# Kernel tuning notes

Hardware: AMD Instinct MI355X
Metric: run time of the kernel (lower is better)

## Reference

```python
import jax, jax.numpy as jnp
import numpy as np

DIMS = 2048
HEADS = 16
HEAD_DIM = DIMS // HEADS  # 128
WIN = 256
THETA = 10000.0


def rotate_half(x):
    x1, x2 = jnp.split(x, 2, axis=-1)
    return jnp.concatenate([-x2, x1], axis=-1)


def rope_freqs(seq_len):
    inv_freq = 1.0 / (THETA ** (jnp.arange(0, HEAD_DIM, 2, dtype=jnp.float32) / HEAD_DIM))
    f = jnp.outer(jnp.arange(seq_len, dtype=jnp.float32), inv_freq)  # [S, D/2]
    return jnp.concatenate([f, f], axis=-1)[None, :, None, :]  # [1, S, 1, D]


def setup_inputs() -> dict:
    key = jax.random.key(0)
    ks = jax.random.split(key, 5)
    B, S = 2, 8192
    scale = 1.0 / np.sqrt(DIMS).astype(np.float32)
    return {
        "hidden_states": jax.random.normal(ks[0], (B, S, DIMS), jnp.float32),
        "Wq": jax.random.normal(ks[1], (DIMS, DIMS), jnp.float32) * scale,
        "Wk": jax.random.normal(ks[2], (DIMS, DIMS), jnp.float32) * scale,
        "Wv": jax.random.normal(ks[3], (DIMS, DIMS), jnp.float32) * scale,
        "Wo": jax.random.normal(ks[4], (DIMS, DIMS), jnp.float32) * scale,
    }


def reference(hidden_states, Wq, Wk, Wv, Wo):
    B, S, _ = hidden_states.shape
    # projections (weights stored [in, out])
    q = (hidden_states @ Wq).reshape(B, S, HEADS, HEAD_DIM)
    k = (hidden_states @ Wk).reshape(B, S, HEADS, HEAD_DIM)
    v = (hidden_states @ Wv).reshape(B, S, HEADS, HEAD_DIM)

    freqs = rope_freqs(S)
    cos, sin = jnp.cos(freqs), jnp.sin(freqs)
    q = q * cos + rotate_half(q) * sin
    k = k * cos + rotate_half(k) * sin

    C = S // WIN
    qc = q.reshape(B, C, WIN, HEADS, HEAD_DIM)
    kc = k.reshape(B, C, WIN, HEADS, HEAD_DIM)
    vc = v.reshape(B, C, WIN, HEADS, HEAD_DIM)

    # previous chunk's K/V (zeros for chunk 0; masked out anyway)
    kp = jnp.concatenate([jnp.zeros_like(kc[:, :1]), kc[:, :-1]], axis=1)
    vp = jnp.concatenate([jnp.zeros_like(vc[:, :1]), vc[:, :-1]], axis=1)
    kcat = jnp.concatenate([kp, kc], axis=2)  # [B, C, 2W, H, D]
    vcat = jnp.concatenate([vp, vc], axis=2)

    scores = jnp.einsum('bcqhd,bckhd->bchqk', qc, kcat) / np.float32(np.sqrt(HEAD_DIM))

    causal = jnp.tril(jnp.ones((WIN, WIN), dtype=bool))  # current-chunk causal
    prev_ok = (jnp.arange(C) > 0)[:, None, None]  # chunk 0 has no previous chunk
    mask = jnp.concatenate([
        jnp.broadcast_to(prev_ok, (C, WIN, WIN)),
        jnp.broadcast_to(causal[None], (C, WIN, WIN)),
    ], axis=-1)  # [C, W, 2W]

    scores = jnp.where(mask[None, :, None], scores, -jnp.inf)
    probs = jax.nn.softmax(scores, axis=-1)
    out = jnp.einsum('bchqk,bckhd->bcqhd', probs, vcat)
    out = out.reshape(B, S, DIMS)
    return out @ Wo
```

## Files before the change

### kernel.cpp

```cpp
#include <hip/hip_runtime.h>
#include <cmath>

#define DIMS 2048
#define SEQ  8192
#define NB   2
#define HEADS 16
#define HD   128
#define WINW 256
#define MROWS 16384
#define NCH  32

using bf16x8 = __attribute__((ext_vector_type(8))) short;
using f32x4  = __attribute__((ext_vector_type(4))) float;

__device__ __forceinline__ unsigned short f2bf(float f) {
  unsigned int u = __float_as_uint(f);
  u += 0x7FFF + ((u >> 16) & 1);
  return (unsigned short)(u >> 16);
}

__device__ __forceinline__ void async16(const unsigned short* g, unsigned short* l) {
  __builtin_amdgcn_global_load_lds((const __attribute__((address_space(1))) void*)g,
                                   (__attribute__((address_space(3))) void*)l,
                                   16, 0, 0);
}

#define BAR() __builtin_amdgcn_s_barrier()
#define WAIT_LGKM0() do { asm volatile("s_waitcnt lgkmcnt(0)" ::: "memory"); \
                          __builtin_amdgcn_sched_barrier(0); } while (0)
#define WAIT_LGKM(n) do { asm volatile("s_waitcnt lgkmcnt(" #n ")" ::: "memory"); \
                          __builtin_amdgcn_sched_barrier(0); } while (0)
#define ORDER() asm volatile("" ::: "memory")
#define WAIT_VM(n) asm volatile("s_waitcnt vmcnt(" #n ")" ::: "memory")
#define MFMA16(a, b, c) __builtin_amdgcn_mfma_f32_16x16x32_bf16(a, b, c, 0, 0, 0)

__global__ __launch_bounds__(256) void prep(
    const float* __restrict__ w0, const float* __restrict__ w1,
    const float* __restrict__ w2, const float* __restrict__ w3,
    const float* __restrict__ H,
    unsigned short* __restrict__ Wt, unsigned short* __restrict__ Hb,
    float* __restrict__ cosT, float* __restrict__ sinT) {
  __shared__ unsigned short tile[64][65];
  const int bid = blockIdx.x;
  const int t = threadIdx.x;
  if (bid < 4096) {
    const int z = bid & 3;
    const int rest = bid >> 2;
    const int n0 = (rest & 31) * 64, k0 = (rest >> 5) * 64;
    const float* W = (z == 0) ? w0 : (z == 1) ? w1 : (z == 2) ? w2 : w3;
    unsigned short* O = Wt + (size_t)z * DIMS * DIMS;
    #pragma unroll
    for (int p = 0; p < 16; ++p) {
      int i = p * 4 + (t >> 6);
      int j = t & 63;
      tile[i][j] = f2bf(W[(size_t)(k0 + i) * DIMS + n0 + j]);
    }
    __syncthreads();
    #pragma unroll
    for (int p = 0; p < 16; ++p) {
      int a = p * 4 + (t >> 6);
      int b = t & 63;
      O[(size_t)(n0 + a) * DIMS + k0 + b] = tile[b][a];
    }
  } else if (bid < 6144) {
    const long n4 = (long)MROWS * DIMS / 4;
    long i = (long)(bid - 4096) * 256 + t;
    for (; i < n4; i += 524288) {
      float4 v = ((const float4*)H)[i];
      ushort4 o;
      o.x = f2bf(v.x); o.y = f2bf(v.y); o.z = f2bf(v.z); o.w = f2bf(v.w);
      ((ushort4*)Hb)[i] = o;
    }
  } else {
    int tl = (bid - 6144) * 256 + t;
    int pos = tl >> 6, i = tl & 63;
    float inv = powf(10000.0f, -(float)i / 64.0f);
    float ang = (float)pos * inv;
    float s, cc;
    __sincosf(ang, &s, &cc);
    cosT[tl] = cc;
    sinT[tl] = s;
  }
}

template<int MODE>
__global__ __launch_bounds__(512, 2) void gemm256(
    const unsigned short* __restrict__ A,
    const unsigned short* __restrict__ WtAll,
    unsigned short* __restrict__ OutB,
    float* __restrict__ OutF,
    const float* __restrict__ cosT,
    const float* __restrict__ sinT) {
  __shared__ __align__(1024) unsigned short lds[65536];
  unsigned short* const As0 = lds;
  unsigned short* const Bs0 = lds + 16384;
  unsigned short* const As1 = lds + 32768;
  unsigned short* const Bs1 = lds + 49152;

  const int tid = threadIdx.x;
  const int wid = tid >> 6, lane = tid & 63;
  const int lo = lane & 15, hi = lane >> 4;
  const int wm = wid >> 2, wn = wid & 3;
  const int flip = (lo & 7) << 4;

  const int nwg = gridDim.x;
  const int orig = blockIdx.x;
  const int bid = (orig & 7) * (nwg >> 3) + (orig >> 3);

  int by, bx, z;
  if (MODE == 0) {
    z = bid >> 9;
    by = (bid & 511) >> 3;
    bx = bid & 7;
  } else {
    by = bid >> 3; bx = bid & 7; z = 3;
  }
  const int m0 = by * 256, n0 = bx * 256;
  const unsigned short* const Ag = A;
  const unsigned short* const Bg = WtAll + (size_t)z * DIMS * DIMS;

  f32x4 acc[8][4];
  #pragma unroll
  for (int i = 0; i < 8; ++i)
    #pragma unroll
    for (int j = 0; j < 4; ++j)
      acc[i][j] = (f32x4){0.f, 0.f, 0.f, 0.f};

  auto stage_half = [&](const unsigned short* __restrict__ G, int grow0, int tile,
                        unsigned short* dst) {
    const int k0 = tile * 64;
    #pragma unroll
    for (int h8 = 0; h8 < 2; ++h8) {
      const int c = h8 * 8 + wid;
      const int row = c * 8 + (lane >> 3);
      const int col8 = (lane & 7) ^ (lane >> 3);
      async16(G + (size_t)(grow0 + row) * DIMS + k0 + col8 * 8, dst + c * 512);
    }
  };
  auto rdA = [&](const unsigned short* base, int i, int kk) -> bf16x8 {
    const int r = i * 32 + wm * 16 + lo;
    const int cb = (kk * 64 + hi * 16) ^ flip;
    return *(const bf16x8*)((const char*)base + r * 128 + cb);
  };
  auto rdB = [&](const unsigned short* base, int j, int kk) -> bf16x8 {
    const int r = j * 64 + wn * 16 + lo;
    const int cb = (kk * 64 + hi * 16) ^ flip;
    return *(const bf16x8*)((const char*)base + r * 128 + cb);
  };

  bf16x8 aq[4][2], b0[2][2], b1[2][2];

  stage_half(Ag, m0,       0, As0);
  stage_half(Bg, n0,       0, Bs0);
  stage_half(Ag, m0 + 128, 0, As0 + 8192);
  stage_half(Bg, n0 + 128, 0, Bs0 + 8192);
  stage_half(Ag, m0,       1, As1);
  stage_half(Bg, n0,       1, Bs1);
  stage_half(Bg, n0 + 128, 1, Bs1 + 8192);
  WAIT_VM(6);
  BAR();

  #pragma unroll 1
  for (int it = 0; it < 16; ++it) {
    const int t = 2 * it;
    const bool pre = (it < 15);
    #pragma unroll
    for (int i = 0; i < 4; ++i) aq[i][0] = rdA(As0, i, 0);
    #pragma unroll
    for (int j = 0; j < 2; ++j) b0[j][0] = rdB(Bs0, j, 0);
    ORDER();
    #pragma unroll
    for (int i = 0; i < 4; ++i) aq[i][1] = rdA(As0, i, 1);
    #pragma unroll
    for (int j = 0; j < 2; ++j) b0[j][1] = rdB(Bs0, j, 1);
    stage_half(Ag, m0 + 128, t + 1, As1 + 8192);
    WAIT_LGKM(6);
    __builtin_amdgcn_s_setprio(1);
    #pragma unroll
    for (int i = 0; i < 4; ++i)
      #pragma unroll
      for (int j = 0; j < 2; ++j)
        acc[i][j] = MFMA16(aq[i][0], b0[j][0], acc[i][j]);
    WAIT_LGKM0();
    #pragma unroll
    for (int i = 0; i < 4; ++i)
      #pragma unroll
      for (int j = 0; j < 2; ++j)
        acc[i][j] = MFMA16(aq[i][1], b0[j][1], acc[i][j]);
    __builtin_amdgcn_s_setprio(0);
    BAR();
    #pragma unroll
    for (int j = 0; j < 2; ++j) b1[j][0] = rdB(Bs0, 2 + j, 0);
    ORDER();
    #pragma unroll
    for (int j = 0; j < 2; ++j) b1[j][1] = rdB(Bs0, 2 + j, 1);
    if (pre) stage_half(Ag, m0, t + 2, As0);
    WAIT_LGKM(2);
    __builtin_amdgcn_s_setprio(1);
    #pragma unroll
    for (int i = 0; i < 4; ++i)
      #pragma unroll
      for (int j = 0; j < 2; ++j)
        acc[i][2 + j] = MFMA16(aq[i][0], b1[j][0], acc[i][2 + j]);
    WAIT_LGKM0();
    #pragma unroll
    for (int i = 0; i < 4; ++i)
      #pragma unroll
      for (int j = 0; j < 2; ++j)
        acc[i][2 + j] = MFMA16(aq[i][1], b1[j][1], acc[i][2 + j]);
    __builtin_amdgcn_s_setprio(0);
    BAR();
    #pragma unroll
    for (int i = 0; i < 4; ++i) aq[i][0] = rdA(As0, 4 + i, 0);
    ORDER();
    #pragma unroll
    for (int i = 0; i < 4; ++i) aq[i][1] = rdA(As0, 4 + i, 1);
    if (pre) stage_half(Bg, n0, t + 2, Bs0);
    WAIT_LGKM(4);
    __builtin_amdgcn_s_setprio(1);
    #pragma unroll
    for (int i = 0; i < 4; ++i)
      #pragma unroll
      for (int j = 0; j < 2; ++j)
        acc[4 + i][j] = MFMA16(aq[i][0], b0[j][0], acc[4 + i][j]);
    WAIT_LGKM0();
    #pragma unroll
    for (int i = 0; i < 4; ++i)
      #pragma unroll
      for (int j = 0; j < 2; ++j)
        acc[4 + i][j] = MFMA16(aq[i][1], b0[j][1], acc[4 + i][j]);
    __builtin_amdgcn_s_setprio(0);
    BAR();
    if (pre) stage_half(Bg, n0 + 128, t + 2, Bs0 + 8192);
    __builtin_amdgcn_s_setprio(1);
    #pragma unroll
    for (int kk = 0; kk < 2; ++kk)
      #pragma unroll
      for (int i = 0; i < 4; ++i)
        #pragma unroll
        for (int j = 0; j < 2; ++j)
          acc[4 + i][2 + j] = MFMA16(aq[i][kk], b1[j][kk], acc[4 + i][2 + j]);
    __builtin_amdgcn_s_setprio(0);
    if (it == 15) { WAIT_VM(0); } else { WAIT_VM(6); }
    BAR();
    #pragma unroll
    for (int i = 0; i < 4; ++i) aq[i][0] = rdA(As1, i, 0);
    #pragma unroll
    for (int j = 0; j < 2; ++j) b0[j][0] = rdB(Bs1, j, 0);
    ORDER();
    #pragma unroll
    for (int i = 0; i < 4; ++i) aq[i][1] = rdA(As1, i, 1);
    #pragma unroll
    for (int j = 0; j < 2; ++j) b0[j][1] = rdB(Bs1, j, 1);
    if (pre) stage_half(Ag, m0 + 128, t + 2, As0 + 8192);
    WAIT_LGKM(6);
    __builtin_amdgcn_s_setprio(1);
    #pragma unroll
    for (int i = 0; i < 4; ++i)
      #pragma unroll
      for (int j = 0; j < 2; ++j)
        acc[i][j] = MFMA16(aq[i][0], b0[j][0], acc[i][j]);
    WAIT_LGKM0();
    #pragma unroll
    for (int i = 0; i < 4; ++i)
      #pragma unroll
      for (int j = 0; j < 2; ++j)
        acc[i][j] = MFMA16(aq[i][1], b0[j][1], acc[i][j]);
    __builtin_amdgcn_s_setprio(0);
    BAR();
    #pragma unroll
    for (int j = 0; j < 2; ++j) b1[j][0] = rdB(Bs1, 2 + j, 0);
    ORDER();
    #pragma unroll
    for (int j = 0; j < 2; ++j) b1[j][1] = rdB(Bs1, 2 + j, 1);
    if (pre) stage_half(Ag, m0, t + 3, As1);
    WAIT_LGKM(2);
    __builtin_amdgcn_s_setprio(1);
    #pragma unroll
    for (int i = 0; i < 4; ++i)
      #pragma unroll
      for (int j = 0; j < 2; ++j)
        acc[i][2 + j] = MFMA16(aq[i][0], b1[j][0], acc[i][2 + j]);
    WAIT_LGKM0();
    #pragma unroll
    for (int i = 0; i < 4; ++i)
      #pragma unroll
      for (int j = 0; j < 2; ++j)
        acc[i][2 + j] = MFMA16(aq[i][1], b1[j][1], acc[i][2 + j]);
    __builtin_amdgcn_s_setprio(0);
    BAR();
    #pragma unroll
    for (int i = 0; i < 4; ++i) aq[i][0] = rdA(As1, 4 + i, 0);
    ORDER();
    #pragma unroll
    for (int i = 0; i < 4; ++i) aq[i][1] = rdA(As1, 4 + i, 1);
    if (pre) stage_half(Bg, n0, t + 3, Bs1);
    WAIT_LGKM(4);
    __builtin_amdgcn_s_setprio(1);
    #pragma unroll
    for (int i = 0; i < 4; ++i)
      #pragma unroll
      for (int j = 0; j < 2; ++j)
        acc[4 + i][j] = MFMA16(aq[i][0], b0[j][0], acc[4 + i][j]);
    WAIT_LGKM0();
    #pragma unroll
    for (int i = 0; i < 4; ++i)
      #pragma unroll
      for (int j = 0; j < 2; ++j)
        acc[4 + i][j] = MFMA16(aq[i][1], b0[j][1], acc[4 + i][j]);
    __builtin_amdgcn_s_setprio(0);
    BAR();
    if (pre) stage_half(Bg, n0 + 128, t + 3, Bs1 + 8192);
    __builtin_amdgcn_s_setprio(1);
    #pragma unroll
    for (int kk = 0; kk < 2; ++kk)
      #pragma unroll
      for (int i = 0; i < 4; ++i)
        #pragma unroll
        for (int j = 0; j < 2; ++j)
          acc[4 + i][2 + j] = MFMA16(aq[i][kk], b1[j][kk], acc[4 + i][2 + j]);
    __builtin_amdgcn_s_setprio(0);
    WAIT_VM(6);
    BAR();
  }

  if (MODE == 0 && z == 2) {
    unsigned short* vt = OutB + (size_t)2 * MROWS * DIMS;
    #pragma unroll
    for (int i = 0; i < 8; ++i) {
      const int row0 = m0 + i * 32 + wm * 16 + hi * 4;
      const int bb = row0 >> 13;
      const int s0 = row0 & (SEQ - 1);
      #pragma unroll
      for (int j = 0; j < 4; ++j) {
        const int colg = n0 + j * 64 + wn * 16 + lo;
        ushort4 pk;
        pk.x = f2bf(acc[i][j][0]); pk.y = f2bf(acc[i][j][1]);
        pk.z = f2bf(acc[i][j][2]); pk.w = f2bf(acc[i][j][3]);
        *(ushort4*)&vt[(((size_t)(bb * 2048 + colg)) << 13) + s0] = pk;
      }
    }
  } else {
    unsigned short* outb = (MODE == 0) ? (OutB + (size_t)z * MROWS * DIMS)
                                       : (unsigned short*)nullptr;
    #pragma unroll
    for (int i = 0; i < 8; ++i) {
      #pragma unroll
      for (int rr = 0; rr < 4; ++rr) {
        const int row = m0 + i * 32 + wm * 16 + hi * 4 + rr;
        const int s = row & (SEQ - 1);
        if (MODE == 1) {
          float* o = OutF + (size_t)row * DIMS + n0;
          #pragma unroll
          for (int j = 0; j < 4; ++j) o[j * 64 + wn * 16 + lo] = acc[i][j][rr];
        } else {
          unsigned short* o = outb + (size_t)row * DIMS + n0;
          const int d = wn * 16 + lo;
          const float cc = cosT[s * 64 + d], sn = sinT[s * 64 + d];
          #pragma unroll
          for (int p = 0; p < 2; ++p) {
            const float v1 = acc[i][2 * p][rr], v2 = acc[i][2 * p + 1][rr];
            o[p * 128 + d]      = f2bf(v1 * cc - v2 * sn);
            o[p * 128 + d + 64] = f2bf(v2 * cc + v1 * sn);
          }
        }
      }
    }
  }
}

__global__ __launch_bounds__(256, 2) void attn(
    const unsigned short* __restrict__ Qb,
    const unsigned short* __restrict__ Kb,
    const unsigned short* __restrict__ Vt,
    unsigned short* __restrict__ AO) {
  __shared__ unsigned short Ksm[2][64 * 128];
  __shared__ unsigned short Vsm[2][128 * 64];
  __shared__ unsigned short Psm[4 * 32 * 64];

  const int nwg = gridDim.x;
  const int orig = blockIdx.x;
  const int bid = (orig & 7) * (nwg >> 3) + (orig >> 3);

  const int qh = bid & 1;
  const int h = (bid >> 1) & 15;
  const int c = (bid >> 5) & 31;
  const int b = bid >> 10;
  const int tid = threadIdx.x;
  const int wid = tid >> 6, lane = tid & 63;
  const int lo = lane & 15, hi = lane >> 4;
  const float SCALE = 0.08838834764831845f;

  const int qbase = qh * 128 + wid * 32;

  bf16x8 qf[2][4];
  {
    const size_t base = ((size_t)(b * SEQ + c * WINW + qbase + lo)) * DIMS + h * HD;
    #pragma unroll
    for (int m = 0; m < 2; ++m)
      #pragma unroll
      for (int ks = 0; ks < 4; ++ks)
        qf[m][ks] = *(const bf16x8*)&Qb[base + (size_t)m * 16 * DIMS + ks * 32 + hi * 8];
  }

  f32x4 O[2][8];
  float mrow[2][4], lrow[2][4];
  #pragma unroll
  for (int m = 0; m < 2; ++m) {
    #pragma unroll
    for (int n = 0; n < 8; ++n) O[m][n] = (f32x4){0.f, 0.f, 0.f, 0.f};
    #pragma unroll
    for (int r = 0; r < 4; ++r) { mrow[m][r] = -INFINITY; lrow[m][r] = 0.f; }
  }

  unsigned short* Pw = Psm + wid * 32 * 64;
  const int t0 = (c == 0) ? 4 : 0;
  const int tend = 5 + 2 * qh;

  const unsigned short* Kg0 = Kb + ((size_t)(b * SEQ + (c - 1) * WINW)) * DIMS + h * HD;
  const unsigned short* Vg0 = Vt + (((size_t)(b * 2048 + h * HD)) << 13) + (c - 1) * WINW;

  auto stageKV = [&](int t, int pb) {
    #pragma unroll
    for (int p = 0; p < 4; ++p) {
      const int cid = p * 256 + tid;
      const int row = cid >> 4, c16 = cid & 15;
      async16(Kg0 + (size_t)(t * 64 + row) * DIMS + ((c16 ^ (row & 7)) << 3),
              &Ksm[pb][cid * 8]);
    }
    #pragma unroll
    for (int p = 0; p < 4; ++p) {
      const int cid = p * 256 + tid;
      const int rd = cid >> 3, c8 = cid & 7;
      async16(Vg0 + ((size_t)rd << 13) + t * 64 + ((c8 ^ (rd & 7)) << 3),
              &Vsm[pb][cid * 8]);
    }
  };

  stageKV(t0, t0 & 1);
  for (int t = t0; t <= tend; ++t) {
    const int pb = t & 1;
    if (t < tend) { stageKV(t + 1, pb ^ 1); WAIT_VM(8); } else { WAIT_VM(0); }
    BAR();

    const bool active = (t < 4) || (((t - 4) << 6) <= qbase + 31);
    if (active) {
      f32x4 S[2][4];
      #pragma unroll
      for (int m = 0; m < 2; ++m)
        #pragma unroll
        for (int n = 0; n < 4; ++n)
          S[m][n] = (f32x4){0.f, 0.f, 0.f, 0.f};
      const char* Kbase = (const char*)&Ksm[pb][0];
      #pragma unroll
      for (int ks = 0; ks < 4; ++ks) {
        bf16x8 kf[4];
        #pragma unroll
        for (int n = 0; n < 4; ++n)
          kf[n] = *(const bf16x8*)(Kbase + (n * 16 + lo) * 256 +
                                   (((ks * 4 + hi) ^ (lo & 7)) << 4));
        #pragma unroll
        for (int m = 0; m < 2; ++m)
          #pragma unroll
          for (int n = 0; n < 4; ++n)
            S[m][n] = MFMA16(qf[m][ks], kf[n], S[m][n]);
      }

      float tmax[2][4];
      #pragma unroll
      for (int m = 0; m < 2; ++m) {
        #pragma unroll
        for (int r = 0; r < 4; ++r) {
          const int qrow = qbase + m * 16 + hi * 4 + r;
          float tm = -INFINITY;
          #pragma unroll
          for (int n = 0; n < 4; ++n) {
            const int kc = t * 64 + n * 16 + lo;
            float v = S[m][n][r] * SCALE;
            const bool ok = (kc < WINW) ? (c > 0) : ((kc - WINW) <= qrow);
            v = ok ? v : -INFINITY;
            S[m][n][r] = v;
            tm = fmaxf(tm, v);
          }
          tm = fmaxf(tm, __shfl_xor(tm, 1));
          tm = fmaxf(tm, __shfl_xor(tm, 2));
          tm = fmaxf(tm, __shfl_xor(tm, 4));
          tm = fmaxf(tm, __shfl_xor(tm, 8));
          tmax[m][r] = tm;
        }
      }
      float need = -INFINITY;
      #pragma unroll
      for (int m = 0; m < 2; ++m)
        #pragma unroll
        for (int r = 0; r < 4; ++r)
          need = fmaxf(need, tmax[m][r] - mrow[m][r]);
      const bool fast = __all(need <= 8.0f);

      #pragma unroll
      for (int m = 0; m < 2; ++m) {
        #pragma unroll
        for (int r = 0; r < 4; ++r) {
          float mused = mrow[m][r];
          if (!fast) {
            mused = fmaxf(mused, tmax[m][r]);
            const float corr = __expf(mrow[m][r] - mused);
            lrow[m][r] *= corr;
            #pragma unroll
            for (int n = 0; n < 8; ++n) O[m][n][r] *= corr;
            mrow[m][r] = mused;
          }
          float rsum = 0.f;
          #pragma unroll
          for (int n = 0; n < 4; ++n) {
            const float p = __expf(S[m][n][r] - mused);
            S[m][n][r] = p;
            rsum += p;
          }
          rsum += __shfl_xor(rsum, 1);
          rsum += __shfl_xor(rsum, 2);
          rsum += __shfl_xor(rsum, 4);
          rsum += __shfl_xor(rsum, 8);
          lrow[m][r] += rsum;
          const int q = m * 16 + hi * 4 + r;
          #pragma unroll
          for (int n = 0; n < 4; ++n) {
            const int boff = (q << 7) + (((n * 16 + lo) << 1) ^ ((q & 7) << 4));
            *(unsigned short*)((char*)Pw + boff) = f2bf(S[m][n][r]);
          }
        }
      }
      asm volatile("" ::: "memory");

      const char* Vbase = (const char*)&Vsm[pb][0];
      #pragma unroll
      for (int kk = 0; kk < 2; ++kk) {
        bf16x8 pf[2], vf[8];
        #pragma unroll
        for (int m = 0; m < 2; ++m) {
          const int q = m * 16 + lo;
          pf[m] = *(const bf16x8*)((const char*)Pw + (q << 7) +
                                   (((kk * 4 + hi) << 4) ^ ((q & 7) << 4)));
        }
        #pragma unroll
        for (int n = 0; n < 8; ++n)
          vf[n] = *(const bf16x8*)(Vbase + (n * 16 + lo) * 128 +
                                   (((kk * 4 + hi) ^ (lo & 7)) << 4));
        #pragma unroll
        for (int m = 0; m < 2; ++m)
          #pragma unroll
          for (int n = 0; n < 8; ++n)
            O[m][n] = MFMA16(pf[m], vf[n], O[m][n]);
      }
    }
    BAR();
  }

  #pragma unroll
  for (int m = 0; m < 2; ++m) {
    #pragma unroll
    for (int r = 0; r < 4; ++r) {
      const float inv = 1.f / lrow[m][r];
      const size_t row = (size_t)(b * SEQ + c * WINW + qbase + m * 16 + hi * 4 + r);
      unsigned short* o = AO + row * DIMS + h * HD;
      #pragma unroll
      for (int n = 0; n < 8; ++n)
        o[n * 16 + lo] = f2bf(O[m][n][r] * inv);
    }
  }
}

extern "C" void kernel_launch(void* const* d_in, const int* in_sizes, int n_in,
                              void* d_out, int out_size, void* d_ws, size_t ws_size,
                              hipStream_t stream) {
  const float* H  = (const float*)d_in[0];
  const float* Wq = (const float*)d_in[1];
  const float* Wk = (const float*)d_in[2];
  const float* Wv = (const float*)d_in[3];
  const float* Wo = (const float*)d_in[4];
  float* out = (float*)d_out;

  unsigned short* Wt  = (unsigned short*)d_ws;
  unsigned short* Hb  = Wt + (size_t)4 * DIMS * DIMS;
  unsigned short* QKV = Hb + (size_t)MROWS * DIMS;
  unsigned short* AO  = QKV + (size_t)3 * MROWS * DIMS;
  float* cosT = (float*)(AO + (size_t)MROWS * DIMS);
  float* sinT = cosT + (size_t)SEQ * 64;

  prep<<<8192, 256, 0, stream>>>(Wq, Wk, Wv, Wo, H, Wt, Hb, cosT, sinT);
  gemm256<0><<<1536, 512, 0, stream>>>(Hb, Wt, QKV, nullptr, cosT, sinT);
  attn<<<2048, 256, 0, stream>>>(QKV, QKV + (size_t)MROWS * DIMS,
                                 QKV + (size_t)2 * MROWS * DIMS, AO);
  gemm256<1><<<512, 512, 0, stream>>>(AO, Wt, nullptr, out, cosT, sinT);
}
```

Measured before the change: 707.8 us.

## Merge query halves into one 512-thread attention block per chunk-head

The attention kernel now handles all 256 query rows of a chunk/head with 8 waves in a single 512-thread workgroup, replacing two 256-thread workgroups that each staged the same K/V tiles. This halves K/V global loads and LDS staging per chunk-head. The blockIdx swizzle is removed, and the P buffer switches from XOR swizzling to a padded stride of 72. The trade-offs are longer per-block runtime, imbalance because waves with early query rows skip work while others still wait at barriers, and possibly lower occupancy from the larger LDS footprint and launch bounds.

```diff
diff --git a/kernel.cpp b/kernel.cpp
--- a/kernel.cpp
+++ b/kernel.cpp
@@ -369,33 +369,27 @@
   }
 }
 
-__global__ __launch_bounds__(256, 2) void attn(
+__global__ __launch_bounds__(512) void attn(
     const unsigned short* __restrict__ Qb,
     const unsigned short* __restrict__ Kb,
     const unsigned short* __restrict__ Vt,
     unsigned short* __restrict__ AO) {
   __shared__ unsigned short Ksm[2][64 * 128];
   __shared__ unsigned short Vsm[2][128 * 64];
-  __shared__ unsigned short Psm[4 * 32 * 64];
-
-  const int nwg = gridDim.x;
-  const int orig = blockIdx.x;
-  const int bid = (orig & 7) * (nwg >> 3) + (orig >> 3);
-
-  const int qh = bid & 1;
-  const int h = (bid >> 1) & 15;
-  const int c = (bid >> 5) & 31;
-  const int b = bid >> 10;
+  __shared__ unsigned short Psm[8 * 32 * 72];
+
+  const int bid = blockIdx.x;
+  const int h = bid & 15;
+  const int c = (bid >> 4) & 31;
+  const int b = bid >> 9;
   const int tid = threadIdx.x;
   const int wid = tid >> 6, lane = tid & 63;
   const int lo = lane & 15, hi = lane >> 4;
   const float SCALE = 0.08838834764831845f;
 
-  const int qbase = qh * 128 + wid * 32;
-
   bf16x8 qf[2][4];
   {
-    const size_t base = ((size_t)(b * SEQ + c * WINW + qbase + lo)) * DIMS + h * HD;
+    const size_t base = ((size_t)(b * SEQ + c * WINW + wid * 32 + lo)) * DIMS + h * HD;
     #pragma unroll
     for (int m = 0; m < 2; ++m)
       #pragma unroll
@@ -413,24 +407,23 @@
     for (int r = 0; r < 4; ++r) { mrow[m][r] = -INFINITY; lrow[m][r] = 0.f; }
   }
 
-  unsigned short* Pw = Psm + wid * 32 * 64;
+  unsigned short* Pw = Psm + wid * 32 * 72;
   const int t0 = (c == 0) ? 4 : 0;
-  const int tend = 5 + 2 * qh;
 
   const unsigned short* Kg0 = Kb + ((size_t)(b * SEQ + (c - 1) * WINW)) * DIMS + h * HD;
   const unsigned short* Vg0 = Vt + (((size_t)(b * 2048 + h * HD)) << 13) + (c - 1) * WINW;
 
   auto stageKV = [&](int t, int pb) {
     #pragma unroll
-    for (int p = 0; p < 4; ++p) {
-      const int cid = p * 256 + tid;
+    for (int p = 0; p < 2; ++p) {
+      const int cid = p * 512 + tid;
       const int row = cid >> 4, c16 = cid & 15;
       async16(Kg0 + (size_t)(t * 64 + row) * DIMS + ((c16 ^ (row & 7)) << 3),
               &Ksm[pb][cid * 8]);
     }
     #pragma unroll
-    for (int p = 0; p < 4; ++p) {
-      const int cid = p * 256 + tid;
+    for (int p = 0; p < 2; ++p) {
+      const int cid = p * 512 + tid;
       const int rd = cid >> 3, c8 = cid & 7;
       async16(Vg0 + ((size_t)rd << 13) + t * 64 + ((c8 ^ (rd & 7)) << 3),
               &Vsm[pb][cid * 8]);
@@ -438,12 +431,12 @@
   };
 
   stageKV(t0, t0 & 1);
-  for (int t = t0; t <= tend; ++t) {
+  for (int t = t0; t < 8; ++t) {
     const int pb = t & 1;
-    if (t < tend) { stageKV(t + 1, pb ^ 1); WAIT_VM(8); } else { WAIT_VM(0); }
-    BAR();
-
-    const bool active = (t < 4) || (((t - 4) << 6) <= qbase + 31);
+    if (t < 7) { stageKV(t + 1, pb ^ 1); WAIT_VM(4); } else { WAIT_VM(0); }
+    BAR();
+
+    const bool active = (t < 4) || (((t - 4) << 6) <= wid * 32 + 31);
     if (active) {
       f32x4 S[2][4];
       #pragma unroll
@@ -471,7 +464,7 @@
       for (int m = 0; m < 2; ++m) {
         #pragma unroll
         for (int r = 0; r < 4; ++r) {
-          const int qrow = qbase + m * 16 + hi * 4 + r;
+          const int qrow = wid * 32 + m * 16 + hi * 4 + r;
           float tm = -INFINITY;
           #pragma unroll
           for (int n = 0; n < 4; ++n) {
@@ -522,12 +515,9 @@
           rsum += __shfl_xor(rsum, 4);
           rsum += __shfl_xor(rsum, 8);
           lrow[m][r] += rsum;
-          const int q = m * 16 + hi * 4 + r;
-          #pragma unroll
-          for (int n = 0; n < 4; ++n) {
-            const int boff = (q << 7) + (((n * 16 + lo) << 1) ^ ((q & 7) << 4));
-            *(unsigned short*)((char*)Pw + boff) = f2bf(S[m][n][r]);
-          }
+          #pragma unroll
+          for (int n = 0; n < 4; ++n)
+            Pw[(m * 16 + hi * 4 + r) * 72 + n * 16 + lo] = f2bf(S[m][n][r]);
         }
       }
       asm volatile("" ::: "memory");
@@ -535,13 +525,11 @@
       const char* Vbase = (const char*)&Vsm[pb][0];
       #pragma unroll
       for (int kk = 0; kk < 2; ++kk) {
+        const int ko = kk * 32 + hi * 8;
         bf16x8 pf[2], vf[8];
         #pragma unroll
-        for (int m = 0; m < 2; ++m) {
-          const int q = m * 16 + lo;
-          pf[m] = *(const bf16x8*)((const char*)Pw + (q << 7) +
-                                   (((kk * 4 + hi) << 4) ^ ((q & 7) << 4)));
-        }
+        for (int m = 0; m < 2; ++m)
+          pf[m] = *(const bf16x8*)&Pw[(m * 16 + lo) * 72 + ko];
         #pragma unroll
         for (int n = 0; n < 8; ++n)
           vf[n] = *(const bf16x8*)(Vbase + (n * 16 + lo) * 128 +
@@ -561,7 +549,7 @@
     #pragma unroll
     for (int r = 0; r < 4; ++r) {
       const float inv = 1.f / lrow[m][r];
-      const size_t row = (size_t)(b * SEQ + c * WINW + qbase + m * 16 + hi * 4 + r);
+      const size_t row = (size_t)(b * SEQ + c * WINW + wid * 32 + m * 16 + hi * 4 + r);
       unsigned short* o = AO + row * DIMS + h * HD;
       #pragma unroll
       for (int n = 0; n < 8; ++n)
@@ -589,7 +577,7 @@
 
   prep<<<8192, 256, 0, stream>>>(Wq, Wk, Wv, Wo, H, Wt, Hb, cosT, sinT);
   gemm256<0><<<1536, 512, 0, stream>>>(Hb, Wt, QKV, nullptr, cosT, sinT);
-  attn<<<2048, 256, 0, stream>>>(QKV, QKV + (size_t)MROWS * DIMS,
-                                 QKV + (size_t)2 * MROWS * DIMS, AO);
+  attn<<<dim3(1024), 512, 0, stream>>>(QKV, QKV + (size_t)MROWS * DIMS,
+                                       QKV + (size_t)2 * MROWS * DIMS, AO);
   gemm256<1><<<512, 512, 0, stream>>>(AO, Wt, nullptr, out, cosT, sinT);
 }
```

Result: no change. 697.4 us, median of 2 (-1.5%).
